# Performance work log

Hardware: AMD Instinct MI355X
Metric: run time of the kernel (lower is better)

The kernel has to match this reference:

```python
import jax, jax.numpy as jnp
import numpy as np

B, S, D = 2, 2048, 1024
H, A = 16, 64  # num_heads, attention_dim


def setup_inputs() -> dict:
    key = jax.random.key(0)
    ks = jax.random.split(key, 9)
    sd = D ** -0.5
    so = (H * A) ** -0.5
    return {
        "x": jax.random.normal(ks[0], (B, S, D), dtype=jnp.float32),
        "Wq": jax.random.normal(ks[1], (D, H * A), dtype=jnp.float32) * sd,
        "bq": jnp.zeros((H * A,), dtype=jnp.float32),
        "Wk": jax.random.normal(ks[2], (D, H * A), dtype=jnp.float32) * sd,
        "bk": jnp.zeros((H * A,), dtype=jnp.float32),
        "Wv": jax.random.normal(ks[3], (D, H * A), dtype=jnp.float32) * sd,
        "bv": jnp.zeros((H * A,), dtype=jnp.float32),
        "Wo": jax.random.normal(ks[4], (H * A, D), dtype=jnp.float32) * so,
        "bo": jnp.zeros((D,), dtype=jnp.float32),
    }


def reference(x, Wq, bq, Wk, bk, Wv, bv, Wo, bo):
    b, s, _ = x.shape
    # project and split heads: [b, s, H, A]
    q = (x @ Wq + bq).reshape(b, s, H, A)
    k = (x @ Wk + bk).reshape(b, s, H, A)
    v = (x @ Wv + bv).reshape(b, s, H, A)
    # scores [b, H, s, s]
    scores = jnp.einsum("bqhd,bkhd->bhqk", q, k) / jnp.sqrt(jnp.float32(A))
    weights = jax.nn.softmax(scores, axis=-1)
    attended = jnp.einsum("bhqk,bkhd->bqhd", weights, v).reshape(b, s, H * A)
    return attended @ Wo + bo
```

## Files before the change

### kernel.cpp

```cpp
#include <hip/hip_runtime.h>
#include <hip/hip_bf16.h>

typedef __attribute__((ext_vector_type(8))) short bf16x8;
typedef __attribute__((ext_vector_type(4))) float f32x4;

#define LOG2E 1.44269504088896f

extern "C" __device__ float __ocml_native_exp2_f32(float);

__device__ __forceinline__ unsigned short f2bf(float f) {
    union { float f; unsigned int u; } v; v.f = f;
    unsigned int r = v.u + 0x7FFF + ((v.u >> 16) & 1);
    return (unsigned short)(r >> 16);
}

__device__ __forceinline__ unsigned int pk_bf16(float lo, float hi) {
    unsigned int r;
    asm("v_cvt_pk_bf16_f32 %0, %1, %2" : "=v"(r) : "v"(lo), "v"(hi));
    return r;
}

typedef __attribute__((address_space(3))) unsigned int lds_uint;
typedef __attribute__((address_space(1))) const unsigned int glob_uint;
__device__ __forceinline__ void gl2lds16(const void* g, void* l) {
    __builtin_amdgcn_global_load_lds((glob_uint*)g, (lds_uint*)l, 16, 0, 0);
}

__global__ __launch_bounds__(256) void cvt_bf16(const float* __restrict__ in,
                                                unsigned int* __restrict__ out, int n4) {
    int i = blockIdx.x * 256 + threadIdx.x;
    if (i >= n4) return;
    float4 v = ((const float4*)in)[i];
    uint2 o;
    o.x = pk_bf16(v.x, v.y);
    o.y = pk_bf16(v.z, v.w);
    ((uint2*)out)[i] = o;
}

__global__ __launch_bounds__(256) void transpose4_bf16(
    const float* __restrict__ w0, const float* __restrict__ w1,
    const float* __restrict__ w2, const float* __restrict__ w3,
    unsigned short* __restrict__ o0, unsigned short* __restrict__ o1,
    unsigned short* __restrict__ o2, unsigned short* __restrict__ o3) {
    const int z = blockIdx.z;
    const float* in = (z == 0) ? w0 : (z == 1) ? w1 : (z == 2) ? w2 : w3;
    unsigned short* out = (z == 0) ? o0 : (z == 1) ? o1 : (z == 2) ? o2 : o3;
    __shared__ float t[32][33];
    int tx = threadIdx.x & 31, ty = threadIdx.x >> 5;
    int r0 = blockIdx.y * 32, c0 = blockIdx.x * 32;
    for (int i = 0; i < 32; i += 8)
        t[ty + i][tx] = in[(size_t)(r0 + ty + i) * 1024 + c0 + tx];
    __syncthreads();
    for (int i = 0; i < 32; i += 8)
        out[(size_t)(c0 + ty + i) * 1024 + r0 + tx] = f2bf(t[tx][ty + i]);
}

__device__ __forceinline__ void gemm_core(const short* __restrict__ A,
                                          const short* __restrict__ BT,
                                          int K, int bm0, int bn0,
                                          short* sm, f32x4 acc[4][4]) {
    const int tid = threadIdx.x;
    const int lane = tid & 63;
    const int w = tid >> 6;
    const int wr0 = (w >> 1) * 64;
    const int wc0 = (w & 1) * 64;
    const int l15 = lane & 15, quad = lane >> 4;
    const int sr = lane >> 2;
    const int slog = (lane & 3) ^ (sr & 3) ^ (sr >> 2);

#pragma unroll
    for (int i = 0; i < 4; i++)
#pragma unroll
        for (int j = 0; j < 4; j++) acc[i][j] = (f32x4)0.f;

    const short* sp[4];
    int sdo[4];
#pragma unroll
    for (int i = 0; i < 4; i++) {
        int c = w * 4 + i;
        sp[i] = (c < 8) ? A + (size_t)(bm0 + c * 16 + sr) * K + slog * 8
                        : BT + (size_t)(bn0 + (c - 8) * 16 + sr) * K + slog * 8;
        sdo[i] = c * 512;
    }
    auto stage = [&](int buf) {
        short* bb = sm + buf * 8192;
#pragma unroll
        for (int i = 0; i < 4; i++) {
            gl2lds16(sp[i], bb + sdo[i]);
            sp[i] += 32;
        }
    };
    const int ph = (quad ^ (l15 & 3) ^ (l15 >> 2)) * 8;
    auto compute = [&](int buf) {
        const short* Ab = sm + buf * 8192;
        const short* Bb = Ab + 4096;
        bf16x8 af[4], bfr[4];
#pragma unroll
        for (int im = 0; im < 4; im++)
            af[im] = *(const bf16x8*)&Ab[(wr0 + im * 16 + l15) * 32 + ph];
#pragma unroll
        for (int in = 0; in < 4; in++)
            bfr[in] = *(const bf16x8*)&Bb[(wc0 + in * 16 + l15) * 32 + ph];
        __builtin_amdgcn_s_setprio(1);
#pragma unroll
        for (int im = 0; im < 4; im++)
#pragma unroll
            for (int in = 0; in < 4; in++)
                acc[im][in] = __builtin_amdgcn_mfma_f32_16x16x32_bf16(af[im], bfr[in], acc[im][in], 0, 0, 0);
        __builtin_amdgcn_s_setprio(0);
    };

    stage(0); stage(1);
    asm volatile("s_waitcnt vmcnt(4)" ::: "memory");
    __builtin_amdgcn_s_barrier();
    asm volatile("" ::: "memory");

    const int nt = K >> 5;
    int bs = 2, bc = 0;
    for (int t = 0; t < nt - 2; ++t) {
        stage(bs); bs = (bs == 2) ? 0 : bs + 1;
        compute(bc); bc = (bc == 2) ? 0 : bc + 1;
        asm volatile("s_waitcnt vmcnt(4)" ::: "memory");
        __builtin_amdgcn_s_barrier();
        asm volatile("" ::: "memory");
    }
    compute(bc); bc = (bc == 2) ? 0 : bc + 1;
    asm volatile("s_waitcnt vmcnt(0)" ::: "memory");
    __builtin_amdgcn_s_barrier();
    asm volatile("" ::: "memory");
    compute(bc);
}

__global__ __launch_bounds__(256) void gemm_qkv(
    const short* __restrict__ xb,
    const short* __restrict__ wqT, const short* __restrict__ wkT, const short* __restrict__ wvT,
    const float* __restrict__ bq, const float* __restrict__ bk, const float* __restrict__ bv,
    unsigned short* __restrict__ qb, unsigned short* __restrict__ kb, unsigned short* __restrict__ vTb) {
    __shared__ short sm[24576];
    const int z = blockIdx.z;
    const short* Amat = (z == 2) ? wvT : xb;
    const short* Bmat = (z == 0) ? wqT : (z == 1) ? wkT : xb;
    const float* bias = (z == 0) ? bq : (z == 1) ? bk : bv;
    const float scl = (z == 0) ? 0.125f * LOG2E : 1.f;
    const int bm0 = (z == 2) ? blockIdx.y * 128 : blockIdx.x * 128;
    const int bn0 = (z == 2) ? blockIdx.x * 128 : blockIdx.y * 128;
    f32x4 acc[4][4];
    gemm_core(Amat, Bmat, 1024, bm0, bn0, sm, acc);
    const int lane = threadIdx.x & 63, w = threadIdx.x >> 6;
    const int wr0 = (w >> 1) * 64, wc0 = (w & 1) * 64, l15 = lane & 15, quad = lane >> 4;
    if (z == 2) {
        for (int im = 0; im < 4; im++)
            for (int in = 0; in < 4; in++)
                for (int r = 0; r < 4; r++) {
                    int rowa = bm0 + wr0 + im * 16 + quad * 4 + r;
                    int colg = bn0 + wc0 + in * 16 + l15;
                    unsigned short ov = f2bf(acc[im][in][r] + bias[rowa]);
                    int b = colg >> 11, s = colg & 2047;
                    vTb[(size_t)b * 2097152 + (size_t)rowa * 2048 + s] = ov;
                }
    } else {
        for (int im = 0; im < 4; im++)
            for (int in = 0; in < 4; in++)
                for (int r = 0; r < 4; r++) {
                    int rowg = bm0 + wr0 + im * 16 + quad * 4 + r;
                    int colg = bn0 + wc0 + in * 16 + l15;
                    unsigned short ov = f2bf((acc[im][in][r] + bias[colg]) * scl);
                    int b = rowg >> 11, s = rowg & 2047;
                    int h = colg >> 6, a = colg & 63;
                    int bh = b * 16 + h;
                    if (z == 0) qb[((size_t)bh * 2048 + s) * 64 + a] = ov;
                    else        kb[((size_t)bh * 2048 + s) * 64 + a] = ov;
                }
    }
}

__global__ __launch_bounds__(256) void gemm_out(
    const short* __restrict__ att, const short* __restrict__ woT,
    const float* __restrict__ bo, float* __restrict__ out) {
    __shared__ short sm[24576];
    const int bm0 = blockIdx.x * 128, bn0 = blockIdx.y * 128;
    f32x4 acc[4][4];
    gemm_core(att, woT, 1024, bm0, bn0, sm, acc);
    const int lane = threadIdx.x & 63, w = threadIdx.x >> 6;
    const int wr0 = (w >> 1) * 64, wc0 = (w & 1) * 64, l15 = lane & 15, quad = lane >> 4;
    for (int im = 0; im < 4; im++)
        for (int in = 0; in < 4; in++)
            for (int r = 0; r < 4; r++) {
                int rowg = bm0 + wr0 + im * 16 + quad * 4 + r;
                int colg = bn0 + wc0 + in * 16 + l15;
                out[(size_t)rowg * 1024 + colg] = acc[im][in][r] + bo[colg];
            }
}

__global__ __launch_bounds__(256, 2) void flash_attn(
    const unsigned short* __restrict__ qb, const unsigned short* __restrict__ kb,
    const unsigned short* __restrict__ vTb, unsigned short* __restrict__ att) {
    __shared__ short Qs[8192];
    __shared__ short Ks[4][4096];
    __shared__ short Vs[4][4096];
    const int tid = threadIdx.x, lane = tid & 63, w = tid >> 6;
    const int l15 = lane & 15, quad = lane >> 4;
    const int q0 = blockIdx.x * 128;
    const int bh = blockIdx.y;
    const size_t qkbase = (size_t)bh * 2048 * 64;
    const size_t vbase = (size_t)bh * 64 * 2048;
    const int sr = lane >> 3;
    const int slog = (lane & 7) ^ sr;
    const int l7 = l15 & 7;

    const unsigned short* sgp;
    int sgstep, sgr;
    short* sgb;
    if (w < 2) {
        sgp = kb + qkbase + (size_t)(w * 32 + sr) * 64 + slog * 8;
        sgstep = 4096;
        sgr = 512;
        sgb = &Ks[0][0] + w * 2048;
    } else {
        sgp = vTb + vbase + (size_t)((w - 2) * 32 + sr) * 2048 + slog * 8;
        sgstep = 64;
        sgr = 16384;
        sgb = &Vs[0][0] + (w - 2) * 2048;
    }
    auto stage_tile = [&](int buf) {
        short* sd = sgb + buf * 4096;
        gl2lds16(sgp, sd);
        gl2lds16(sgp + sgr, sd + 512);
        gl2lds16(sgp + 2 * sgr, sd + 1024);
        gl2lds16(sgp + 3 * sgr, sd + 1536);
        sgp += sgstep;
    };

#pragma unroll
    for (int i = 0; i < 4; i++) {
        int c = w * 4 + i;
        gl2lds16(qb + qkbase + (size_t)(q0 + c * 8 + sr) * 64 + slog * 8, Qs + c * 512);
    }
    stage_tile(0); stage_tile(1); stage_tile(2);
    asm volatile("s_waitcnt vmcnt(8)" ::: "memory");
    __builtin_amdgcn_s_barrier();
    asm volatile("" ::: "memory");

    const int wq0 = w * 32;
    const int c0 = (quad ^ l7) * 8, c1 = c0 ^ 32;
    const int fb = l15 * 64;
    bf16x8 aq00 = *(const bf16x8*)&Qs[(wq0 + l15) * 64 + c0];
    bf16x8 aq01 = *(const bf16x8*)&Qs[(wq0 + l15) * 64 + c1];
    bf16x8 aq10 = *(const bf16x8*)&Qs[(wq0 + 16 + l15) * 64 + c0];
    bf16x8 aq11 = *(const bf16x8*)&Qs[(wq0 + 16 + l15) * 64 + c1];

    f32x4 o0[4], o1[4];
#pragma unroll
    for (int dt = 0; dt < 4; dt++) { o0[dt] = (f32x4)0.f; o1[dt] = (f32x4)0.f; }
    f32x4 ls0 = (f32x4)0.f, ls1 = (f32x4)0.f;

    auto smax = [&](f32x4 (&sc)[4], f32x4& lsr, bf16x8 (&bp)[2]) {
#pragma unroll
        for (int t = 0; t < 4; t++) {
#pragma unroll
            for (int r = 0; r < 4; r++) sc[t][r] = __ocml_native_exp2_f32(sc[t][r]);
            lsr += sc[t];
        }
#pragma unroll
        for (int t2 = 0; t2 < 2; t2++) {
            unsigned pa = pk_bf16(sc[2 * t2][0], sc[2 * t2][1]);
            unsigned pb = pk_bf16(sc[2 * t2][2], sc[2 * t2][3]);
            unsigned pc = pk_bf16(sc[2 * t2 + 1][0], sc[2 * t2 + 1][1]);
            unsigned pd = pk_bf16(sc[2 * t2 + 1][2], sc[2 * t2 + 1][3]);
            asm("v_permlane32_swap_b32 %0, %1" : "+v"(pa), "+v"(pc));
            asm("v_permlane32_swap_b32 %0, %1" : "+v"(pb), "+v"(pd));
            asm("v_permlane16_swap_b32 %0, %1" : "+v"(pa), "+v"(pc));
            asm("v_permlane16_swap_b32 %0, %1" : "+v"(pb), "+v"(pd));
            union { unsigned u[4]; bf16x8 v; } cvt;
            cvt.u[0] = pa; cvt.u[1] = pb; cvt.u[2] = pc; cvt.u[3] = pd;
            bp[t2] = cvt.v;
        }
    };

    auto attn_step = [&](int buf) {
        const short* Kb = &Ks[0][0] + buf * 4096;
        const short* Vb = &Vs[0][0] + buf * 4096;
        f32x4 sc0[4], sc1[4];
        __builtin_amdgcn_s_setprio(1);
#pragma unroll
        for (int t = 0; t < 4; t++) {
            bf16x8 ak = *(const bf16x8*)(Kb + fb + c0 + t * 1024);
            sc0[t] = __builtin_amdgcn_mfma_f32_16x16x32_bf16(ak, aq00, (f32x4)0.f, 0, 0, 0);
            sc1[t] = __builtin_amdgcn_mfma_f32_16x16x32_bf16(ak, aq10, (f32x4)0.f, 0, 0, 0);
        }
#pragma unroll
        for (int t = 0; t < 4; t++) {
            bf16x8 ak = *(const bf16x8*)(Kb + fb + c1 + t * 1024);
            sc0[t] = __builtin_amdgcn_mfma_f32_16x16x32_bf16(ak, aq01, sc0[t], 0, 0, 0);
            sc1[t] = __builtin_amdgcn_mfma_f32_16x16x32_bf16(ak, aq11, sc1[t], 0, 0, 0);
        }
        __builtin_amdgcn_s_setprio(0);
        bf16x8 bp0[2], bp1[2];
        smax(sc0, ls0, bp0);
        smax(sc1, ls1, bp1);
        __builtin_amdgcn_s_setprio(1);
#pragma unroll
        for (int t2 = 0; t2 < 2; t2++) {
            const int cc = t2 ? c1 : c0;
#pragma unroll
            for (int dt = 0; dt < 4; dt++) {
                bf16x8 av = *(const bf16x8*)(Vb + fb + cc + dt * 1024);
                o0[dt] = __builtin_amdgcn_mfma_f32_16x16x32_bf16(av, bp0[t2], o0[dt], 0, 0, 0);
                o1[dt] = __builtin_amdgcn_mfma_f32_16x16x32_bf16(av, bp1[t2], o1[dt], 0, 0, 0);
            }
        }
        __builtin_amdgcn_s_setprio(0);
    };

    for (int t = 0; t < 29; t++) {
        stage_tile((t + 3) & 3);
        attn_step(t & 3);
        asm volatile("s_waitcnt vmcnt(8)" ::: "memory");
        __builtin_amdgcn_s_barrier();
        asm volatile("" ::: "memory");
    }
    attn_step(1);
    asm volatile("s_waitcnt vmcnt(4)" ::: "memory");
    __builtin_amdgcn_s_barrier();
    asm volatile("" ::: "memory");
    attn_step(2);
    asm volatile("s_waitcnt vmcnt(0)" ::: "memory");
    __builtin_amdgcn_s_barrier();
    asm volatile("" ::: "memory");
    attn_step(3);

    const int b = bh >> 4, h = bh & 15;
    float l0 = (ls0[0] + ls0[1]) + (ls0[2] + ls0[3]);
    l0 += __shfl_xor(l0, 16);
    l0 += __shfl_xor(l0, 32);
    float inv0 = 1.f / l0;
    float l1 = (ls1[0] + ls1[1]) + (ls1[2] + ls1[3]);
    l1 += __shfl_xor(l1, 16);
    l1 += __shfl_xor(l1, 32);
    float inv1 = 1.f / l1;
    int s = q0 + wq0 + l15;
#pragma unroll
    for (int dt = 0; dt < 4; dt++) {
        int col = h * 64 + dt * 16 + quad * 4;
        uint2 pk;
        pk.x = pk_bf16(o0[dt][0] * inv0, o0[dt][1] * inv0);
        pk.y = pk_bf16(o0[dt][2] * inv0, o0[dt][3] * inv0);
        *(uint2*)&att[((size_t)b * 2048 + s) * 1024 + col] = pk;
        pk.x = pk_bf16(o1[dt][0] * inv1, o1[dt][1] * inv1);
        pk.y = pk_bf16(o1[dt][2] * inv1, o1[dt][3] * inv1);
        *(uint2*)&att[((size_t)b * 2048 + s + 16) * 1024 + col] = pk;
    }
}

extern "C" void kernel_launch(void* const* d_in, const int* in_sizes, int n_in,
                              void* d_out, int out_size, void* d_ws, size_t ws_size,
                              hipStream_t stream) {
    const float* x  = (const float*)d_in[0];
    const float* Wq = (const float*)d_in[1];
    const float* bq = (const float*)d_in[2];
    const float* Wk = (const float*)d_in[3];
    const float* bk = (const float*)d_in[4];
    const float* Wv = (const float*)d_in[5];
    const float* bv = (const float*)d_in[6];
    const float* Wo = (const float*)d_in[7];
    const float* bo = (const float*)d_in[8];
    float* out = (float*)d_out;

    short* ws  = (short*)d_ws;
    short* xb  = ws;
    short* wqT = ws + 4 * 1024 * 1024;
    short* wkT = wqT + 1024 * 1024;
    short* wvT = wkT + 1024 * 1024;
    short* woT = wvT + 1024 * 1024;
    short* qb  = woT + 1024 * 1024;
    short* kb  = qb + 4 * 1024 * 1024;
    short* vTb = kb + 4 * 1024 * 1024;
    short* att = vTb + 4 * 1024 * 1024;

    cvt_bf16<<<4096, 256, 0, stream>>>(x, (unsigned int*)xb, 1024 * 1024);
    transpose4_bf16<<<dim3(32, 32, 4), 256, 0, stream>>>(
        Wq, Wk, Wv, Wo,
        (unsigned short*)wqT, (unsigned short*)wkT,
        (unsigned short*)wvT, (unsigned short*)woT);
    gemm_qkv<<<dim3(32, 8, 3), 256, 0, stream>>>(xb, wqT, wkT, wvT, bq, bk, bv,
                                                 (unsigned short*)qb, (unsigned short*)kb,
                                                 (unsigned short*)vTb);
    flash_attn<<<dim3(16, 32), 256, 0, stream>>>((const unsigned short*)qb,
                                                 (const unsigned short*)kb,
                                                 (const unsigned short*)vTb,
                                                 (unsigned short*)att);
    gemm_out<<<dim3(32, 8), 256, 0, stream>>>(att, woT, bo, out);
}
```

Baseline: 185.5 us.

## Register double-buffer LDS fragments in GEMM and attention loops; load Q directly

Both the GEMM core and the flash-attention loop now read the next tile's LDS fragments into a second register set before issuing the MFMAs on the current set, unrolling by two so LDS reads overlap matrix math. Waits at each barrier now also drain LDS counters. The GEMM kernels get an occupancy hint of three blocks per CU, and flash attention drops the Q shared-memory staging in favour of direct global loads into registers. The cost is higher register pressure from the doubled fragment buffers, which may cause spills or conflict with the occupancy hint. The buffer-index bookkeeping in the reordered pipeline is also intricate.

```diff
diff --git a/kernel.cpp b/kernel.cpp
--- a/kernel.cpp
+++ b/kernel.cpp
@@ -25,6 +25,11 @@
 __device__ __forceinline__ void gl2lds16(const void* g, void* l) {
     __builtin_amdgcn_global_load_lds((glob_uint*)g, (lds_uint*)l, 16, 0, 0);
 }
+
+#define SYNC(vm)                                                             \
+    asm volatile("s_waitcnt vmcnt(" #vm ")\n\ts_waitcnt lgkmcnt(0)" ::: "memory"); \
+    __builtin_amdgcn_s_barrier();                                            \
+    asm volatile("" ::: "memory")
 
 __global__ __launch_bounds__(256) void cvt_bf16(const float* __restrict__ in,
                                                 unsigned int* __restrict__ out, int n4) {
@@ -91,16 +96,18 @@
         }
     };
     const int ph = (quad ^ (l15 & 3) ^ (l15 >> 2)) * 8;
-    auto compute = [&](int buf) {
+    auto loadf = [&](bf16x8* af, bf16x8* bfr, int buf) {
         const short* Ab = sm + buf * 8192;
         const short* Bb = Ab + 4096;
-        bf16x8 af[4], bfr[4];
 #pragma unroll
         for (int im = 0; im < 4; im++)
             af[im] = *(const bf16x8*)&Ab[(wr0 + im * 16 + l15) * 32 + ph];
 #pragma unroll
         for (int in = 0; in < 4; in++)
             bfr[in] = *(const bf16x8*)&Bb[(wc0 + in * 16 + l15) * 32 + ph];
+        __builtin_amdgcn_sched_barrier(0);
+    };
+    auto computef = [&](const bf16x8* af, const bf16x8* bfr) {
         __builtin_amdgcn_s_setprio(1);
 #pragma unroll
         for (int im = 0; im < 4; im++)
@@ -115,23 +122,28 @@
     __builtin_amdgcn_s_barrier();
     asm volatile("" ::: "memory");
 
+    bf16x8 aA[4], bA[4], aB[4], bB[4];
+    loadf(aA, bA, 0);
+
     const int nt = K >> 5;
-    int bs = 2, bc = 0;
-    for (int t = 0; t < nt - 2; ++t) {
+    int bs = 2, rb = 1;
+    for (int t = 0; t < nt - 2; t += 2) {
         stage(bs); bs = (bs == 2) ? 0 : bs + 1;
-        compute(bc); bc = (bc == 2) ? 0 : bc + 1;
-        asm volatile("s_waitcnt vmcnt(4)" ::: "memory");
-        __builtin_amdgcn_s_barrier();
-        asm volatile("" ::: "memory");
-    }
-    compute(bc); bc = (bc == 2) ? 0 : bc + 1;
-    asm volatile("s_waitcnt vmcnt(0)" ::: "memory");
-    __builtin_amdgcn_s_barrier();
-    asm volatile("" ::: "memory");
-    compute(bc);
-}
-
-__global__ __launch_bounds__(256) void gemm_qkv(
+        SYNC(4);
+        loadf(aB, bB, rb); rb = (rb == 2) ? 0 : rb + 1;
+        computef(aA, bA);
+        stage(bs); bs = (bs == 2) ? 0 : bs + 1;
+        SYNC(4);
+        loadf(aA, bA, rb); rb = (rb == 2) ? 0 : rb + 1;
+        computef(aB, bB);
+    }
+    SYNC(0);
+    loadf(aB, bB, rb);
+    computef(aA, bA);
+    computef(aB, bB);
+}
+
+__global__ __launch_bounds__(256, 3) void gemm_qkv(
     const short* __restrict__ xb,
     const short* __restrict__ wqT, const short* __restrict__ wkT, const short* __restrict__ wvT,
     const float* __restrict__ bq, const float* __restrict__ bk, const float* __restrict__ bv,
@@ -174,7 +186,7 @@
     }
 }
 
-__global__ __launch_bounds__(256) void gemm_out(
+__global__ __launch_bounds__(256, 3) void gemm_out(
     const short* __restrict__ att, const short* __restrict__ woT,
     const float* __restrict__ bo, float* __restrict__ out) {
     __shared__ short sm[24576];
@@ -195,7 +207,6 @@
 __global__ __launch_bounds__(256, 2) void flash_attn(
     const unsigned short* __restrict__ qb, const unsigned short* __restrict__ kb,
     const unsigned short* __restrict__ vTb, unsigned short* __restrict__ att) {
-    __shared__ short Qs[8192];
     __shared__ short Ks[4][4096];
     __shared__ short Vs[4][4096];
     const int tid = threadIdx.x, lane = tid & 63, w = tid >> 6;
@@ -213,13 +224,11 @@
     short* sgb;
     if (w < 2) {
         sgp = kb + qkbase + (size_t)(w * 32 + sr) * 64 + slog * 8;
-        sgstep = 4096;
-        sgr = 512;
+        sgstep = 4096; sgr = 512;
         sgb = &Ks[0][0] + w * 2048;
     } else {
         sgp = vTb + vbase + (size_t)((w - 2) * 32 + sr) * 2048 + slog * 8;
-        sgstep = 64;
-        sgr = 16384;
+        sgstep = 64; sgr = 16384;
         sgb = &Vs[0][0] + (w - 2) * 2048;
     }
     auto stage_tile = [&](int buf) {
@@ -231,28 +240,38 @@
         sgp += sgstep;
     };
 
-#pragma unroll
-    for (int i = 0; i < 4; i++) {
-        int c = w * 4 + i;
-        gl2lds16(qb + qkbase + (size_t)(q0 + c * 8 + sr) * 64 + slog * 8, Qs + c * 512);
-    }
+    const int wq0 = w * 32;
+    const int c0 = (quad ^ l7) * 8, c1 = c0 ^ 32;
+    const int fb = l15 * 64;
+
+    const unsigned short* qrow = qb + qkbase + (size_t)(q0 + wq0 + l15) * 64 + quad * 8;
+    bf16x8 aq00 = *(const bf16x8*)qrow;
+    bf16x8 aq01 = *(const bf16x8*)(qrow + 32);
+    bf16x8 aq10 = *(const bf16x8*)(qrow + 1024);
+    bf16x8 aq11 = *(const bf16x8*)(qrow + 1024 + 32);
+
     stage_tile(0); stage_tile(1); stage_tile(2);
     asm volatile("s_waitcnt vmcnt(8)" ::: "memory");
     __builtin_amdgcn_s_barrier();
     asm volatile("" ::: "memory");
 
-    const int wq0 = w * 32;
-    const int c0 = (quad ^ l7) * 8, c1 = c0 ^ 32;
-    const int fb = l15 * 64;
-    bf16x8 aq00 = *(const bf16x8*)&Qs[(wq0 + l15) * 64 + c0];
-    bf16x8 aq01 = *(const bf16x8*)&Qs[(wq0 + l15) * 64 + c1];
-    bf16x8 aq10 = *(const bf16x8*)&Qs[(wq0 + 16 + l15) * 64 + c0];
-    bf16x8 aq11 = *(const bf16x8*)&Qs[(wq0 + 16 + l15) * 64 + c1];
-
     f32x4 o0[4], o1[4];
 #pragma unroll
     for (int dt = 0; dt < 4; dt++) { o0[dt] = (f32x4)0.f; o1[dt] = (f32x4)0.f; }
     f32x4 ls0 = (f32x4)0.f, ls1 = (f32x4)0.f;
+
+    auto load_frags = [&](bf16x8* kf, bf16x8* vf, int buf) {
+        const short* Kb = &Ks[0][0] + buf * 4096;
+        const short* Vb = &Vs[0][0] + buf * 4096;
+#pragma unroll
+        for (int t = 0; t < 4; t++) {
+            kf[2 * t]     = *(const bf16x8*)(Kb + fb + c0 + t * 1024);
+            kf[2 * t + 1] = *(const bf16x8*)(Kb + fb + c1 + t * 1024);
+            vf[2 * t]     = *(const bf16x8*)(Vb + fb + c0 + t * 1024);
+            vf[2 * t + 1] = *(const bf16x8*)(Vb + fb + c1 + t * 1024);
+        }
+        __builtin_amdgcn_sched_barrier(0);
+    };
 
     auto smax = [&](f32x4 (&sc)[4], f32x4& lsr, bf16x8 (&bp)[2]) {
 #pragma unroll
@@ -277,22 +296,18 @@
         }
     };
 
-    auto attn_step = [&](int buf) {
-        const short* Kb = &Ks[0][0] + buf * 4096;
-        const short* Vb = &Vs[0][0] + buf * 4096;
+    auto compute_step = [&](const bf16x8* kf, const bf16x8* vf) {
         f32x4 sc0[4], sc1[4];
         __builtin_amdgcn_s_setprio(1);
 #pragma unroll
         for (int t = 0; t < 4; t++) {
-            bf16x8 ak = *(const bf16x8*)(Kb + fb + c0 + t * 1024);
-            sc0[t] = __builtin_amdgcn_mfma_f32_16x16x32_bf16(ak, aq00, (f32x4)0.f, 0, 0, 0);
-            sc1[t] = __builtin_amdgcn_mfma_f32_16x16x32_bf16(ak, aq10, (f32x4)0.f, 0, 0, 0);
+            sc0[t] = __builtin_amdgcn_mfma_f32_16x16x32_bf16(kf[2 * t], aq00, (f32x4)0.f, 0, 0, 0);
+            sc1[t] = __builtin_amdgcn_mfma_f32_16x16x32_bf16(kf[2 * t], aq10, (f32x4)0.f, 0, 0, 0);
         }
 #pragma unroll
         for (int t = 0; t < 4; t++) {
-            bf16x8 ak = *(const bf16x8*)(Kb + fb + c1 + t * 1024);
-            sc0[t] = __builtin_amdgcn_mfma_f32_16x16x32_bf16(ak, aq01, sc0[t], 0, 0, 0);
-            sc1[t] = __builtin_amdgcn_mfma_f32_16x16x32_bf16(ak, aq11, sc1[t], 0, 0, 0);
+            sc0[t] = __builtin_amdgcn_mfma_f32_16x16x32_bf16(kf[2 * t + 1], aq01, sc0[t], 0, 0, 0);
+            sc1[t] = __builtin_amdgcn_mfma_f32_16x16x32_bf16(kf[2 * t + 1], aq11, sc1[t], 0, 0, 0);
         }
         __builtin_amdgcn_s_setprio(0);
         bf16x8 bp0[2], bp1[2];
@@ -300,34 +315,39 @@
         smax(sc1, ls1, bp1);
         __builtin_amdgcn_s_setprio(1);
 #pragma unroll
-        for (int t2 = 0; t2 < 2; t2++) {
-            const int cc = t2 ? c1 : c0;
+        for (int t2 = 0; t2 < 2; t2++)
 #pragma unroll
             for (int dt = 0; dt < 4; dt++) {
-                bf16x8 av = *(const bf16x8*)(Vb + fb + cc + dt * 1024);
-                o0[dt] = __builtin_amdgcn_mfma_f32_16x16x32_bf16(av, bp0[t2], o0[dt], 0, 0, 0);
-                o1[dt] = __builtin_amdgcn_mfma_f32_16x16x32_bf16(av, bp1[t2], o1[dt], 0, 0, 0);
+                o0[dt] = __builtin_amdgcn_mfma_f32_16x16x32_bf16(vf[2 * dt + t2], bp0[t2], o0[dt], 0, 0, 0);
+                o1[dt] = __builtin_amdgcn_mfma_f32_16x16x32_bf16(vf[2 * dt + t2], bp1[t2], o1[dt], 0, 0, 0);
             }
-        }
         __builtin_amdgcn_s_setprio(0);
     };
 
-    for (int t = 0; t < 29; t++) {
+    bf16x8 kA[8], vA[8], kB[8], vB[8];
+    load_frags(kA, vA, 0);
+
+    for (int t = 0; t < 28; t += 2) {
         stage_tile((t + 3) & 3);
-        attn_step(t & 3);
-        asm volatile("s_waitcnt vmcnt(8)" ::: "memory");
-        __builtin_amdgcn_s_barrier();
-        asm volatile("" ::: "memory");
-    }
-    attn_step(1);
-    asm volatile("s_waitcnt vmcnt(4)" ::: "memory");
-    __builtin_amdgcn_s_barrier();
-    asm volatile("" ::: "memory");
-    attn_step(2);
-    asm volatile("s_waitcnt vmcnt(0)" ::: "memory");
-    __builtin_amdgcn_s_barrier();
-    asm volatile("" ::: "memory");
-    attn_step(3);
+        SYNC(8);
+        load_frags(kB, vB, (t + 1) & 3);
+        compute_step(kA, vA);
+        stage_tile((t + 4) & 3);
+        SYNC(8);
+        load_frags(kA, vA, (t + 2) & 3);
+        compute_step(kB, vB);
+    }
+    stage_tile(3);
+    SYNC(8);
+    load_frags(kB, vB, 29 & 3);
+    compute_step(kA, vA);
+    SYNC(4);
+    load_frags(kA, vA, 30 & 3);
+    compute_step(kB, vB);
+    SYNC(0);
+    load_frags(kB, vB, 31 & 3);
+    compute_step(kA, vA);
+    compute_step(kB, vB);
 
     const int b = bh >> 4, h = bh & 15;
     float l0 = (ls0[0] + ls0[1]) + (ls0[2] + ls0[3]);
```

New measurement: 181.5 us. -2.2%, faster.
